# Kernel tuning notes

Measured on AMD Instinct MI355X. Metric: run time of the kernel, lower is better.

The kernel has to match this reference:

```python
import jax, jax.numpy as jnp
import numpy as np

N_NODES = 50000
N_EDGES = 800000
N_GRAPHS = 512
VOCAB = 100000
EMB = 64
HID = 128
CLASSES = 2


def setup_inputs() -> dict:
    key = jax.random.key(0)
    ks = jax.random.split(key, 12)
    x = jax.random.randint(ks[0], (N_NODES,), 0, VOCAB)
    edge_index = jax.random.randint(ks[1], (2, N_EDGES), 0, N_NODES)
    batch = jnp.sort(jax.random.randint(ks[2], (N_NODES,), 0, N_GRAPHS))
    s = lambda fan_in: 1.0 / np.sqrt(fan_in)
    emb_table = jax.random.normal(ks[3], (VOCAB, EMB), jnp.float32)
    w1_l = jax.random.uniform(ks[4], (EMB, HID), jnp.float32, -s(EMB), s(EMB))
    b1 = jnp.zeros((HID,), jnp.float32)
    w1_r = jax.random.uniform(ks[5], (EMB, HID), jnp.float32, -s(EMB), s(EMB))
    w2_l = jax.random.uniform(ks[6], (HID, HID), jnp.float32, -s(HID), s(HID))
    b2 = jnp.zeros((HID,), jnp.float32)
    w2_r = jax.random.uniform(ks[7], (HID, HID), jnp.float32, -s(HID), s(HID))
    w_out = jax.random.uniform(ks[8], (HID, CLASSES), jnp.float32, -s(HID), s(HID))
    b_out = jnp.zeros((CLASSES,), jnp.float32)
    return {"x": x, "edge_index": edge_index, "batch": batch,
            "emb_table": emb_table, "w1_l": w1_l, "b1": b1, "w1_r": w1_r,
            "w2_l": w2_l, "b2": b2, "w2_r": w2_r, "w_out": w_out, "b_out": b_out}


def _sage_conv(h, src, dst, w_l, b_l, w_r):
    # PyG SAGEConv (mean aggr): out = lin_l(mean_{j in N(i)} x_j) + lin_r(x_i)
    msg = h[src]                                              # [E, F] gather
    agg = jax.ops.segment_sum(msg, dst, num_segments=N_NODES)  # [N, F]
    deg = jax.ops.segment_sum(jnp.ones((src.shape[0],), h.dtype), dst,
                              num_segments=N_NODES)
    mean = agg / jnp.maximum(deg, 1.0)[:, None]
    return mean @ w_l + b_l + h @ w_r


def reference(x, edge_index, batch, emb_table, w1_l, b1, w1_r,
              w2_l, b2, w2_r, w_out, b_out):
    src, dst = edge_index[0], edge_index[1]
    h = emb_table[x]                                          # [N, EMB]
    h = jax.nn.relu(_sage_conv(h, src, dst, w1_l, b1, w1_r))
    # dropout is identity in eval mode
    h = jax.nn.relu(_sage_conv(h, src, dst, w2_l, b2, w2_r))
    # global mean pool over graphs
    pooled = jax.ops.segment_sum(h, batch, num_segments=N_GRAPHS)
    cnt = jax.ops.segment_sum(jnp.ones((N_NODES,), h.dtype), batch,
                              num_segments=N_GRAPHS)
    pooled = pooled / jnp.maximum(cnt, 1.0)[:, None]
    return pooled @ w_out + b_out                              # [G, CLASSES]
```

## Files before the change

kernel.cpp:

```cpp
#include <hip/hip_runtime.h>
#include <hip/hip_bf16.h>

#define N_NODES 50000
#define N_EDGES 800000
#define N_GRAPHS 512
#define EMB 64
#define HID 128

__device__ __forceinline__ unsigned f2bf(float f) {
    unsigned x = __float_as_uint(f);
    return (x + 0x7fffu + ((x >> 16) & 1u)) >> 16;
}
__device__ __forceinline__ unsigned packbf(float lo, float hi) {
    return f2bf(lo) | (f2bf(hi) << 16);
}
__device__ __forceinline__ float bf_lo(unsigned u) { return __uint_as_float(u << 16); }
__device__ __forceinline__ float bf_hi(unsigned u) { return __uint_as_float(u & 0xffff0000u); }

__global__ void k_embed_hist(const int* __restrict__ x, const float* __restrict__ emb,
                             const int* __restrict__ ei, float* __restrict__ h0,
                             uint2* __restrict__ h0b, int* __restrict__ deg) {
    int t = blockIdx.x * 256 + threadIdx.x;
    if (t >= N_EDGES) return;
    int n = t >> 4, c4 = t & 15;
    const float4* e4 = (const float4*)emb;
    float4 v = e4[(size_t)x[n] * 16 + c4];
    ((float4*)h0)[(size_t)n * 16 + c4] = v;
    uint2 b; b.x = packbf(v.x, v.y); b.y = packbf(v.z, v.w);
    h0b[(size_t)n * 16 + c4] = b;
    atomicAdd(&deg[ei[N_EDGES + t]], 1);
}

__global__ void k_scanA(const int* __restrict__ deg, int* __restrict__ rowptr,
                        int* __restrict__ bsums) {
    __shared__ int s[256];
    int t = threadIdx.x, i = blockIdx.x * 256 + t;
    int v = (i < N_NODES) ? deg[i] : 0;
    s[t] = v; __syncthreads();
    int xv = v;
    for (int off = 1; off < 256; off <<= 1) {
        int y = (t >= off) ? s[t - off] : 0;
        __syncthreads();
        xv += y; s[t] = xv;
        __syncthreads();
    }
    if (i < N_NODES) rowptr[i] = xv - v;
    if (t == 255) bsums[blockIdx.x] = xv;
}

__global__ void k_scanB(int* __restrict__ bsums, int nb) {
    __shared__ int s[256];
    int t = threadIdx.x;
    int v = (t < nb) ? bsums[t] : 0;
    s[t] = v; __syncthreads();
    int xv = v;
    for (int off = 1; off < 256; off <<= 1) {
        int y = (t >= off) ? s[t - off] : 0;
        __syncthreads();
        xv += y; s[t] = xv;
        __syncthreads();
    }
    if (t < nb) bsums[t] = xv - v;
}

__global__ void k_scanC(int* __restrict__ rowptr, int* __restrict__ wp,
                        const int* __restrict__ bsums) {
    int i = blockIdx.x * 256 + threadIdx.x;
    if (i < N_NODES) {
        int v = rowptr[i] + bsums[blockIdx.x];
        rowptr[i] = v;
        wp[i] = v;
    }
    if (i == 0) rowptr[N_NODES] = N_EDGES;
}

__global__ void k_scatter(const int* __restrict__ ei, int* __restrict__ wp,
                          int* __restrict__ nbr) {
    int e = blockIdx.x * 256 + threadIdx.x;
    if (e >= N_EDGES) return;
    int s = ei[e], d = ei[N_EDGES + e];
    int pos = atomicAdd(&wp[d], 1);
    nbr[pos] = s;
}

template <int F>
__device__ __forceinline__ void agg_tile_bf(const uint2* __restrict__ hb,
                                            const int* __restrict__ rowptr,
                                            const int* __restrict__ nbr,
                                            float* __restrict__ mean,
                                            int aggIdx, int t) {
    int wl = t >> 6;
    int l = t & 63;
    float4* m4 = (float4*)mean;

    int n, c;
    if constexpr (F == 128) { n = aggIdx * 16 + wl * 2 + (l >> 5); c = l & 31; }
    else                    { n = aggIdx * 32 + wl * 4 + (l >> 4); c = l & 15; }
    if (n >= N_NODES) return;
    constexpr int CU2 = F / 4;

    int r0 = rowptr[n], r1 = rowptr[n + 1];
    float inv = 1.0f / (float)max(r1 - r0, 1);

    float4 a[8];
    #pragma unroll
    for (int u = 0; u < 8; ++u) a[u] = make_float4(0.f, 0.f, 0.f, 0.f);

    int i = r0;
    for (; i + 7 < r1; i += 8) {
        int s0 = nbr[i + 0], s1 = nbr[i + 1], s2 = nbr[i + 2], s3 = nbr[i + 3];
        int s4 = nbr[i + 4], s5 = nbr[i + 5], s6 = nbr[i + 6], s7 = nbr[i + 7];
        uint2 v0 = hb[(size_t)s0 * CU2 + c];
        uint2 v1 = hb[(size_t)s1 * CU2 + c];
        uint2 v2 = hb[(size_t)s2 * CU2 + c];
        uint2 v3 = hb[(size_t)s3 * CU2 + c];
        uint2 v4 = hb[(size_t)s4 * CU2 + c];
        uint2 v5 = hb[(size_t)s5 * CU2 + c];
        uint2 v6 = hb[(size_t)s6 * CU2 + c];
        uint2 v7 = hb[(size_t)s7 * CU2 + c];
        a[0].x += bf_lo(v0.x); a[0].y += bf_hi(v0.x); a[0].z += bf_lo(v0.y); a[0].w += bf_hi(v0.y);
        a[1].x += bf_lo(v1.x); a[1].y += bf_hi(v1.x); a[1].z += bf_lo(v1.y); a[1].w += bf_hi(v1.y);
        a[2].x += bf_lo(v2.x); a[2].y += bf_hi(v2.x); a[2].z += bf_lo(v2.y); a[2].w += bf_hi(v2.y);
        a[3].x += bf_lo(v3.x); a[3].y += bf_hi(v3.x); a[3].z += bf_lo(v3.y); a[3].w += bf_hi(v3.y);
        a[4].x += bf_lo(v4.x); a[4].y += bf_hi(v4.x); a[4].z += bf_lo(v4.y); a[4].w += bf_hi(v4.y);
        a[5].x += bf_lo(v5.x); a[5].y += bf_hi(v5.x); a[5].z += bf_lo(v5.y); a[5].w += bf_hi(v5.y);
        a[6].x += bf_lo(v6.x); a[6].y += bf_hi(v6.x); a[6].z += bf_lo(v6.y); a[6].w += bf_hi(v6.y);
        a[7].x += bf_lo(v7.x); a[7].y += bf_hi(v7.x); a[7].z += bf_lo(v7.y); a[7].w += bf_hi(v7.y);
    }
    for (; i + 3 < r1; i += 4) {
        int s0 = nbr[i + 0], s1 = nbr[i + 1], s2 = nbr[i + 2], s3 = nbr[i + 3];
        uint2 v0 = hb[(size_t)s0 * CU2 + c];
        uint2 v1 = hb[(size_t)s1 * CU2 + c];
        uint2 v2 = hb[(size_t)s2 * CU2 + c];
        uint2 v3 = hb[(size_t)s3 * CU2 + c];
        a[0].x += bf_lo(v0.x); a[0].y += bf_hi(v0.x); a[0].z += bf_lo(v0.y); a[0].w += bf_hi(v0.y);
        a[1].x += bf_lo(v1.x); a[1].y += bf_hi(v1.x); a[1].z += bf_lo(v1.y); a[1].w += bf_hi(v1.y);
        a[2].x += bf_lo(v2.x); a[2].y += bf_hi(v2.x); a[2].z += bf_lo(v2.y); a[2].w += bf_hi(v2.y);
        a[3].x += bf_lo(v3.x); a[3].y += bf_hi(v3.x); a[3].z += bf_lo(v3.y); a[3].w += bf_hi(v3.y);
    }
    for (; i < r1; ++i) {
        uint2 v = hb[(size_t)nbr[i] * CU2 + c];
        a[0].x += bf_lo(v.x); a[0].y += bf_hi(v.x); a[0].z += bf_lo(v.y); a[0].w += bf_hi(v.y);
    }
    #pragma unroll
    for (int u = 1; u < 8; ++u) {
        a[0].x += a[u].x; a[0].y += a[u].y; a[0].z += a[u].z; a[0].w += a[u].w;
    }
    m4[(size_t)n * CU2 + c] = make_float4(a[0].x * inv, a[0].y * inv,
                                          a[0].z * inv, a[0].w * inv);
}

template <int K, bool MEAN, bool WB>
__device__ __forceinline__ void gemm_tile(const float* __restrict__ hin,
                                          const float* __restrict__ w,
                                          const float* __restrict__ bias,
                                          float* __restrict__ out,
                                          uint2* __restrict__ outb,
                                          int blk, int t, float* ls) {
    constexpr int LS = K + 2;
    constexpr int C4 = K / 4;
    int base = blk * 64;
    int lane = t & 63;
    int wid = __builtin_amdgcn_readfirstlane(t >> 6);
    int j0 = wid * 16;
    int node = base + lane;
    bool valid = node < N_NODES;

    const float4* h4 = (const float4*)hin;
    for (int idx = t; idx < 64 * C4; idx += 512) {
        int r = idx / C4, c4 = idx % C4;
        float4 v = (base + r < N_NODES) ? h4[(size_t)(base + r) * C4 + c4]
                                        : make_float4(0.f, 0.f, 0.f, 0.f);
        float* dp = &ls[r * LS + c4 * 4];
        dp[0] = v.x; dp[1] = v.y; dp[2] = v.z; dp[3] = v.w;
    }
    __syncthreads();

    float acc[16];
    if constexpr (MEAN) {
        const float4* o4 = (const float4*)out;
        #pragma unroll
        for (int jj = 0; jj < 4; ++jj) {
            float4 v = valid ? o4[(size_t)node * 32 + wid * 4 + jj]
                             : make_float4(0.f, 0.f, 0.f, 0.f);
            acc[jj * 4 + 0] = v.x; acc[jj * 4 + 1] = v.y;
            acc[jj * 4 + 2] = v.z; acc[jj * 4 + 3] = v.w;
        }
    } else {
        #pragma unroll
        for (int j = 0; j < 16; ++j) acc[j] = bias[j0 + j];
    }

    const float* lrow = &ls[lane * LS];
    #pragma unroll 4
    for (int k = 0; k < K; ++k) {
        float hv = lrow[k];
        const float* wk = &w[(size_t)k * 128 + j0];
        #pragma unroll
        for (int j = 0; j < 16; ++j) acc[j] = fmaf(hv, wk[j], acc[j]);
    }

    if (!valid) return;
    float4* o4 = (float4*)out;
    #pragma unroll
    for (int jj = 0; jj < 4; ++jj) {
        float4 v;
        if constexpr (MEAN) {
            v.x = fmaxf(acc[jj * 4 + 0], 0.f);
            v.y = fmaxf(acc[jj * 4 + 1], 0.f);
            v.z = fmaxf(acc[jj * 4 + 2], 0.f);
            v.w = fmaxf(acc[jj * 4 + 3], 0.f);
        } else {
            v.x = acc[jj * 4 + 0]; v.y = acc[jj * 4 + 1];
            v.z = acc[jj * 4 + 2]; v.w = acc[jj * 4 + 3];
        }
        o4[(size_t)node * 32 + wid * 4 + jj] = v;
        if constexpr (WB) {
            uint2 u; u.x = packbf(v.x, v.y); u.y = packbf(v.z, v.w);
            outb[(size_t)node * 32 + wid * 4 + jj] = u;
        }
    }
}

__global__ __launch_bounds__(512) void k_fuse1(
    const float* __restrict__ h0, const uint2* __restrict__ h0b,
    const int* __restrict__ rowptr, const int* __restrict__ nbr,
    float* __restrict__ mean1, const float* __restrict__ w1r,
    const float* __restrict__ b1, float* __restrict__ h1) {
    __shared__ float ls[64 * (64 + 2)];
    int b = blockIdx.x;
    if (b % 3 == 2)
        gemm_tile<64, false, false>(h0, w1r, b1, h1, nullptr, b / 3, threadIdx.x, ls);
    else
        agg_tile_bf<64>(h0b, rowptr, nbr, mean1, (b / 3) * 2 + b % 3, threadIdx.x);
}

__global__ __launch_bounds__(512) void k_fuse2(
    const float* __restrict__ h1, const uint2* __restrict__ h1b,
    const int* __restrict__ rowptr, const int* __restrict__ nbr,
    float* __restrict__ mean2, const float* __restrict__ w2r,
    const float* __restrict__ b2, float* __restrict__ h2) {
    __shared__ float ls[64 * (128 + 2)];
    int b = blockIdx.x;
    if (b % 5 == 4)
        gemm_tile<128, false, false>(h1, w2r, b2, h2, nullptr, b / 5, threadIdx.x, ls);
    else
        agg_tile_bf<128>(h1b, rowptr, nbr, mean2, (b / 5) * 4 + b % 5, threadIdx.x);
}

__global__ __launch_bounds__(512) void k_gemm_mean64(
    const float* __restrict__ mean1, const float* __restrict__ w1l,
    float* __restrict__ h1, uint2* __restrict__ h1b) {
    __shared__ float ls[64 * (64 + 2)];
    gemm_tile<64, true, true>(mean1, w1l, nullptr, h1, h1b, blockIdx.x, threadIdx.x, ls);
}

__global__ __launch_bounds__(512) void k_gemm_mean128(
    const float* __restrict__ mean2, const float* __restrict__ w2l,
    float* __restrict__ h2) {
    __shared__ float ls[64 * (128 + 2)];
    gemm_tile<128, true, false>(mean2, w2l, nullptr, h2, nullptr, blockIdx.x, threadIdx.x, ls);
}

__global__ void k_pool_head(const float* __restrict__ h2, const int* __restrict__ batch,
                            const float* __restrict__ w_out, const float* __restrict__ b_out,
                            float* __restrict__ out) {
    int g = blockIdx.x;
    int lo = 0, hi = N_NODES;
    while (lo < hi) { int mid = (lo + hi) >> 1; if (batch[mid] < g) lo = mid + 1; else hi = mid; }
    int s = lo;
    lo = s; hi = N_NODES;
    while (lo < hi) { int mid = (lo + hi) >> 1; if (batch[mid] < g + 1) lo = mid + 1; else hi = mid; }
    int e = lo;

    int f = threadIdx.x & 127, half = threadIdx.x >> 7;
    float acc = 0.0f;
    for (int r = s + half; r < e; r += 2) acc += h2[(size_t)r * 128 + f];
    __shared__ float tmp[256];
    tmp[threadIdx.x] = acc;
    __syncthreads();
    if (half == 0) {
        float p = (tmp[f] + tmp[f + 128]) / (float)max(e - s, 1);
        tmp[f]       = p * w_out[f * 2 + 0];
        tmp[f + 128] = p * w_out[f * 2 + 1];
    }
    __syncthreads();
    for (int str = 64; str > 0; str >>= 1) {
        if (threadIdx.x < str) {
            tmp[threadIdx.x] += tmp[threadIdx.x + str];
            tmp[threadIdx.x + 128] += tmp[threadIdx.x + 128 + str];
        }
        __syncthreads();
    }
    if (threadIdx.x == 0) {
        out[(size_t)g * 2 + 0] = tmp[0] + b_out[0];
        out[(size_t)g * 2 + 1] = tmp[128] + b_out[1];
    }
}

extern "C" void kernel_launch(void* const* d_in, const int* in_sizes, int n_in,
                              void* d_out, int out_size, void* d_ws, size_t ws_size,
                              hipStream_t stream) {
    const int*   x      = (const int*)d_in[0];
    const int*   ei     = (const int*)d_in[1];
    const int*   batch  = (const int*)d_in[2];
    const float* emb    = (const float*)d_in[3];
    const float* w1_l   = (const float*)d_in[4];
    const float* b1     = (const float*)d_in[5];
    const float* w1_r   = (const float*)d_in[6];
    const float* w2_l   = (const float*)d_in[7];
    const float* b2     = (const float*)d_in[8];
    const float* w2_r   = (const float*)d_in[9];
    const float* w_out  = (const float*)d_in[10];
    const float* b_out  = (const float*)d_in[11];
    float* out = (float*)d_out;

    float* F = (float*)d_ws;
    float* A = F;
    float* B = A + (size_t)N_NODES * 64;
    float* C = B + (size_t)N_NODES * 64;
    float* D = C + (size_t)N_NODES * 128;
    float* h0    = A;
    uint2* h1b   = (uint2*)A;
    float* mean1 = B;
    float* h1    = C;
    float* h2    = C;
    float* mean2 = D;
    uint2* h0b   = (uint2*)D;
    int*   deg   = (int*)(D + (size_t)N_NODES * 128);
    int*   rowptr= deg + N_NODES;
    int*   wp    = rowptr + N_NODES + 1;
    int*   nbr   = wp + N_NODES;
    int*   bsums = nbr + N_EDGES;

    const int NB = (N_NODES + 255) / 256;
    const int GB = (N_NODES + 63) / 64;

    hipMemsetAsync(deg, 0, (size_t)N_NODES * sizeof(int), stream);

    k_embed_hist<<<(N_EDGES + 255) / 256, 256, 0, stream>>>(x, emb, ei, h0, h0b, deg);
    k_scanA<<<NB, 256, 0, stream>>>(deg, rowptr, bsums);
    k_scanB<<<1, 256, 0, stream>>>(bsums, NB);
    k_scanC<<<NB, 256, 0, stream>>>(rowptr, wp, bsums);
    k_scatter<<<(N_EDGES + 255) / 256, 256, 0, stream>>>(ei, wp, nbr);

    k_fuse1<<<3 * GB, 512, 0, stream>>>(h0, h0b, rowptr, nbr, mean1, w1_r, b1, h1);
    k_gemm_mean64<<<GB, 512, 0, stream>>>(mean1, w1_l, h1, h1b);

    k_fuse2<<<5 * GB, 512, 0, stream>>>(h1, h1b, rowptr, nbr, mean2, w2_r, b2, h2);
    k_gemm_mean128<<<GB, 512, 0, stream>>>(mean2, w2_l, h2);

    k_pool_head<<<N_GRAPHS, 256, 0, stream>>>(h2, batch, w_out, b_out, out);

    (void)in_sizes; (void)n_in; (void)out_size; (void)ws_size;
}
```

Measured before the change: 370.2 us.

## Fuse mean-pool into final GEMM and drop fp32 activation copies

Removes the fp32 h0/h1 copies; self-term GEMMs now stage bf16 activations from shared memory. The layer-2 mean GEMM performs ReLU and a per-block segmented column sum into a pooled buffer with atomics, so h2 is never written or reread. The head kernel only normalizes and applies the output linear. This trades slightly lower precision on the root-term input and atomic contention for less global memory traffic.

```diff
diff --git a/kernel.cpp b/kernel.cpp
--- a/kernel.cpp
+++ b/kernel.cpp
@@ -18,14 +18,13 @@
 __device__ __forceinline__ float bf_hi(unsigned u) { return __uint_as_float(u & 0xffff0000u); }
 
 __global__ void k_embed_hist(const int* __restrict__ x, const float* __restrict__ emb,
-                             const int* __restrict__ ei, float* __restrict__ h0,
-                             uint2* __restrict__ h0b, int* __restrict__ deg) {
+                             const int* __restrict__ ei, uint2* __restrict__ h0b,
+                             int* __restrict__ deg) {
     int t = blockIdx.x * 256 + threadIdx.x;
     if (t >= N_EDGES) return;
     int n = t >> 4, c4 = t & 15;
     const float4* e4 = (const float4*)emb;
     float4 v = e4[(size_t)x[n] * 16 + c4];
-    ((float4*)h0)[(size_t)n * 16 + c4] = v;
     uint2 b; b.x = packbf(v.x, v.y); b.y = packbf(v.z, v.w);
     h0b[(size_t)n * 16 + c4] = b;
     atomicAdd(&deg[ei[N_EDGES + t]], 1);
@@ -150,48 +149,38 @@
                                           a[0].z * inv, a[0].w * inv);
 }
 
-template <int K, bool MEAN, bool WB>
-__device__ __forceinline__ void gemm_tile(const float* __restrict__ hin,
-                                          const float* __restrict__ w,
-                                          const float* __restrict__ bias,
-                                          float* __restrict__ out,
-                                          uint2* __restrict__ outb,
-                                          int blk, int t, float* ls) {
-    constexpr int LS = K + 2;
-    constexpr int C4 = K / 4;
-    int base = blk * 64;
-    int lane = t & 63;
-    int wid = __builtin_amdgcn_readfirstlane(t >> 6);
-    int j0 = wid * 16;
-    int node = base + lane;
-    bool valid = node < N_NODES;
-
+template <int K>
+__device__ __forceinline__ void stage_f32(const float* __restrict__ hin, int base,
+                                          int t, float* ls) {
+    constexpr int LS = K + 2, C4 = K / 4;
     const float4* h4 = (const float4*)hin;
     for (int idx = t; idx < 64 * C4; idx += 512) {
-        int r = idx / C4, c4 = idx % C4;
-        float4 v = (base + r < N_NODES) ? h4[(size_t)(base + r) * C4 + c4]
+        int r = idx / C4, c = idx % C4;
+        float4 v = (base + r < N_NODES) ? h4[(size_t)(base + r) * C4 + c]
                                         : make_float4(0.f, 0.f, 0.f, 0.f);
-        float* dp = &ls[r * LS + c4 * 4];
+        float* dp = &ls[r * LS + c * 4];
         dp[0] = v.x; dp[1] = v.y; dp[2] = v.z; dp[3] = v.w;
     }
-    __syncthreads();
-
-    float acc[16];
-    if constexpr (MEAN) {
-        const float4* o4 = (const float4*)out;
-        #pragma unroll
-        for (int jj = 0; jj < 4; ++jj) {
-            float4 v = valid ? o4[(size_t)node * 32 + wid * 4 + jj]
-                             : make_float4(0.f, 0.f, 0.f, 0.f);
-            acc[jj * 4 + 0] = v.x; acc[jj * 4 + 1] = v.y;
-            acc[jj * 4 + 2] = v.z; acc[jj * 4 + 3] = v.w;
-        }
-    } else {
-        #pragma unroll
-        for (int j = 0; j < 16; ++j) acc[j] = bias[j0 + j];
-    }
-
-    const float* lrow = &ls[lane * LS];
+}
+
+template <int K>
+__device__ __forceinline__ void stage_bf(const uint2* __restrict__ hb, int base,
+                                         int t, float* ls) {
+    constexpr int LS = K + 2, C2 = K / 4;
+    for (int idx = t; idx < 64 * C2; idx += 512) {
+        int r = idx / C2, c = idx % C2;
+        uint2 v = (base + r < N_NODES) ? hb[(size_t)(base + r) * C2 + c]
+                                       : make_uint2(0u, 0u);
+        float* dp = &ls[r * LS + c * 4];
+        dp[0] = bf_lo(v.x); dp[1] = bf_hi(v.x);
+        dp[2] = bf_lo(v.y); dp[3] = bf_hi(v.y);
+    }
+}
+
+template <int K>
+__device__ __forceinline__ void gemm_core(const float* __restrict__ lrow,
+                                          const float* __restrict__ w,
+                                          int j0, float (&acc)[16]) {
     #pragma unroll 4
     for (int k = 0; k < K; ++k) {
         float hv = lrow[k];
@@ -199,102 +188,160 @@
         #pragma unroll
         for (int j = 0; j < 16; ++j) acc[j] = fmaf(hv, wk[j], acc[j]);
     }
-
-    if (!valid) return;
-    float4* o4 = (float4*)out;
-    #pragma unroll
-    for (int jj = 0; jj < 4; ++jj) {
-        float4 v;
-        if constexpr (MEAN) {
-            v.x = fmaxf(acc[jj * 4 + 0], 0.f);
-            v.y = fmaxf(acc[jj * 4 + 1], 0.f);
-            v.z = fmaxf(acc[jj * 4 + 2], 0.f);
-            v.w = fmaxf(acc[jj * 4 + 3], 0.f);
-        } else {
-            v.x = acc[jj * 4 + 0]; v.y = acc[jj * 4 + 1];
-            v.z = acc[jj * 4 + 2]; v.w = acc[jj * 4 + 3];
+}
+
+__global__ __launch_bounds__(512) void k_fuse1(
+    const uint2* __restrict__ h0b, const int* __restrict__ rowptr,
+    const int* __restrict__ nbr, float* __restrict__ mean1,
+    const float* __restrict__ w1r, const float* __restrict__ b1,
+    float* __restrict__ pre1) {
+    __shared__ float ls[64 * 66];
+    int b = blockIdx.x, t = threadIdx.x;
+    if (b % 3 == 2) {
+        int base = (b / 3) * 64;
+        stage_bf<64>(h0b, base, t, ls);
+        __syncthreads();
+        int lane = t & 63, wid = __builtin_amdgcn_readfirstlane(t >> 6), j0 = wid * 16;
+        int node = base + lane;
+        float acc[16];
+        #pragma unroll
+        for (int j = 0; j < 16; ++j) acc[j] = b1[j0 + j];
+        gemm_core<64>(&ls[lane * 66], w1r, j0, acc);
+        if (node < N_NODES) {
+            float4* o4 = (float4*)pre1;
+            #pragma unroll
+            for (int jj = 0; jj < 4; ++jj)
+                o4[(size_t)node * 32 + wid * 4 + jj] =
+                    make_float4(acc[jj*4], acc[jj*4+1], acc[jj*4+2], acc[jj*4+3]);
         }
-        o4[(size_t)node * 32 + wid * 4 + jj] = v;
-        if constexpr (WB) {
-            uint2 u; u.x = packbf(v.x, v.y); u.y = packbf(v.z, v.w);
-            outb[(size_t)node * 32 + wid * 4 + jj] = u;
+    } else {
+        agg_tile_bf<64>(h0b, rowptr, nbr, mean1, (b / 3) * 2 + (b % 3), t);
+    }
+}
+
+__global__ __launch_bounds__(512) void k_fuse2(
+    const uint2* __restrict__ h1b, const int* __restrict__ rowptr,
+    const int* __restrict__ nbr, float* __restrict__ mean2,
+    const float* __restrict__ w2r, const float* __restrict__ b2,
+    float* __restrict__ pre2) {
+    __shared__ float ls[64 * 130];
+    int b = blockIdx.x, t = threadIdx.x;
+    if (b % 5 == 4) {
+        int base = (b / 5) * 64;
+        stage_bf<128>(h1b, base, t, ls);
+        __syncthreads();
+        int lane = t & 63, wid = __builtin_amdgcn_readfirstlane(t >> 6), j0 = wid * 16;
+        int node = base + lane;
+        float acc[16];
+        #pragma unroll
+        for (int j = 0; j < 16; ++j) acc[j] = b2[j0 + j];
+        gemm_core<128>(&ls[lane * 130], w2r, j0, acc);
+        if (node < N_NODES) {
+            float4* o4 = (float4*)pre2;
+            #pragma unroll
+            for (int jj = 0; jj < 4; ++jj)
+                o4[(size_t)node * 32 + wid * 4 + jj] =
+                    make_float4(acc[jj*4], acc[jj*4+1], acc[jj*4+2], acc[jj*4+3]);
         }
-    }
-}
-
-__global__ __launch_bounds__(512) void k_fuse1(
-    const float* __restrict__ h0, const uint2* __restrict__ h0b,
-    const int* __restrict__ rowptr, const int* __restrict__ nbr,
-    float* __restrict__ mean1, const float* __restrict__ w1r,
-    const float* __restrict__ b1, float* __restrict__ h1) {
-    __shared__ float ls[64 * (64 + 2)];
-    int b = blockIdx.x;
-    if (b % 3 == 2)
-        gemm_tile<64, false, false>(h0, w1r, b1, h1, nullptr, b / 3, threadIdx.x, ls);
-    else
-        agg_tile_bf<64>(h0b, rowptr, nbr, mean1, (b / 3) * 2 + b % 3, threadIdx.x);
-}
-
-__global__ __launch_bounds__(512) void k_fuse2(
-    const float* __restrict__ h1, const uint2* __restrict__ h1b,
-    const int* __restrict__ rowptr, const int* __restrict__ nbr,
-    float* __restrict__ mean2, const float* __restrict__ w2r,
-    const float* __restrict__ b2, float* __restrict__ h2) {
-    __shared__ float ls[64 * (128 + 2)];
-    int b = blockIdx.x;
-    if (b % 5 == 4)
-        gemm_tile<128, false, false>(h1, w2r, b2, h2, nullptr, b / 5, threadIdx.x, ls);
-    else
-        agg_tile_bf<128>(h1b, rowptr, nbr, mean2, (b / 5) * 4 + b % 5, threadIdx.x);
+    } else {
+        agg_tile_bf<128>(h1b, rowptr, nbr, mean2, (b / 5) * 4 + (b % 5), t);
+    }
 }
 
 __global__ __launch_bounds__(512) void k_gemm_mean64(
     const float* __restrict__ mean1, const float* __restrict__ w1l,
-    float* __restrict__ h1, uint2* __restrict__ h1b) {
-    __shared__ float ls[64 * (64 + 2)];
-    gemm_tile<64, true, true>(mean1, w1l, nullptr, h1, h1b, blockIdx.x, threadIdx.x, ls);
-}
-
-__global__ __launch_bounds__(512) void k_gemm_mean128(
+    const float* __restrict__ pre1, uint2* __restrict__ h1b) {
+    __shared__ float ls[64 * 66];
+    int t = threadIdx.x, base = blockIdx.x * 64;
+    stage_f32<64>(mean1, base, t, ls);
+    __syncthreads();
+    int lane = t & 63, wid = __builtin_amdgcn_readfirstlane(t >> 6), j0 = wid * 16;
+    int node = base + lane;
+    bool valid = node < N_NODES;
+    float acc[16];
+    const float4* p4 = (const float4*)pre1;
+    #pragma unroll
+    for (int jj = 0; jj < 4; ++jj) {
+        float4 v = valid ? p4[(size_t)node * 32 + wid * 4 + jj]
+                         : make_float4(0.f, 0.f, 0.f, 0.f);
+        acc[jj*4] = v.x; acc[jj*4+1] = v.y; acc[jj*4+2] = v.z; acc[jj*4+3] = v.w;
+    }
+    gemm_core<64>(&ls[lane * 66], w1l, j0, acc);
+    if (!valid) return;
+    #pragma unroll
+    for (int jj = 0; jj < 4; ++jj) {
+        float a0 = fmaxf(acc[jj*4+0], 0.f), a1 = fmaxf(acc[jj*4+1], 0.f);
+        float a2 = fmaxf(acc[jj*4+2], 0.f), a3 = fmaxf(acc[jj*4+3], 0.f);
+        uint2 u; u.x = packbf(a0, a1); u.y = packbf(a2, a3);
+        h1b[(size_t)node * 32 + wid * 4 + jj] = u;
+    }
+}
+
+__global__ __launch_bounds__(512) void k_mean128_pool(
     const float* __restrict__ mean2, const float* __restrict__ w2l,
-    float* __restrict__ h2) {
-    __shared__ float ls[64 * (128 + 2)];
-    gemm_tile<128, true, false>(mean2, w2l, nullptr, h2, nullptr, blockIdx.x, threadIdx.x, ls);
-}
-
-__global__ void k_pool_head(const float* __restrict__ h2, const int* __restrict__ batch,
-                            const float* __restrict__ w_out, const float* __restrict__ b_out,
-                            float* __restrict__ out) {
-    int g = blockIdx.x;
+    const float* __restrict__ pre2, const int* __restrict__ batch,
+    float* __restrict__ pooled) {
+    __shared__ float ls[64 * 130];
+    __shared__ int bb[64];
+    int t = threadIdx.x, base = blockIdx.x * 64;
+    stage_f32<128>(mean2, base, t, ls);
+    if (t < 64) bb[t] = (base + t < N_NODES) ? batch[base + t] : -1;
+    __syncthreads();
+    int lane = t & 63, wid = __builtin_amdgcn_readfirstlane(t >> 6), j0 = wid * 16;
+    int node = base + lane;
+    bool valid = node < N_NODES;
+    float acc[16];
+    const float4* p4 = (const float4*)pre2;
+    #pragma unroll
+    for (int jj = 0; jj < 4; ++jj) {
+        float4 v = valid ? p4[(size_t)node * 32 + wid * 4 + jj]
+                         : make_float4(0.f, 0.f, 0.f, 0.f);
+        acc[jj*4] = v.x; acc[jj*4+1] = v.y; acc[jj*4+2] = v.z; acc[jj*4+3] = v.w;
+    }
+    gemm_core<128>(&ls[lane * 130], w2l, j0, acc);
+    __syncthreads();
+    #pragma unroll
+    for (int j = 0; j < 16; ++j)
+        ls[lane * 129 + j0 + j] = valid ? fmaxf(acc[j], 0.f) : 0.f;
+    __syncthreads();
+    if (t < 128) {
+        int col = t;
+        float run = 0.f;
+        int gcur = bb[0];
+        for (int r = 0; r < 64; ++r) {
+            int g = bb[r];
+            if (g != gcur) {
+                if (gcur >= 0) atomicAdd(&pooled[gcur * 128 + col], run);
+                run = 0.f; gcur = g;
+            }
+            run += ls[r * 129 + col];
+        }
+        if (gcur >= 0) atomicAdd(&pooled[gcur * 128 + col], run);
+    }
+}
+
+__global__ void k_head(const float* __restrict__ pooled, const int* __restrict__ batch,
+                       const float* __restrict__ w_out, const float* __restrict__ b_out,
+                       float* __restrict__ out) {
+    int g = blockIdx.x, f = threadIdx.x;
     int lo = 0, hi = N_NODES;
-    while (lo < hi) { int mid = (lo + hi) >> 1; if (batch[mid] < g) lo = mid + 1; else hi = mid; }
+    while (lo < hi) { int m = (lo + hi) >> 1; if (batch[m] < g) lo = m + 1; else hi = m; }
     int s = lo;
     lo = s; hi = N_NODES;
-    while (lo < hi) { int mid = (lo + hi) >> 1; if (batch[mid] < g + 1) lo = mid + 1; else hi = mid; }
-    int e = lo;
-
-    int f = threadIdx.x & 127, half = threadIdx.x >> 7;
-    float acc = 0.0f;
-    for (int r = s + half; r < e; r += 2) acc += h2[(size_t)r * 128 + f];
-    __shared__ float tmp[256];
-    tmp[threadIdx.x] = acc;
+    while (lo < hi) { int m = (lo + hi) >> 1; if (batch[m] < g + 1) lo = m + 1; else hi = m; }
+    int cnt = lo - s;
+    float p = pooled[(size_t)g * 128 + f] / (float)max(cnt, 1);
+    __shared__ float red[256];
+    red[f] = p * w_out[f * 2 + 0];
+    red[128 + f] = p * w_out[f * 2 + 1];
     __syncthreads();
-    if (half == 0) {
-        float p = (tmp[f] + tmp[f + 128]) / (float)max(e - s, 1);
-        tmp[f]       = p * w_out[f * 2 + 0];
-        tmp[f + 128] = p * w_out[f * 2 + 1];
-    }
-    __syncthreads();
-    for (int str = 64; str > 0; str >>= 1) {
-        if (threadIdx.x < str) {
-            tmp[threadIdx.x] += tmp[threadIdx.x + str];
-            tmp[threadIdx.x + 128] += tmp[threadIdx.x + 128 + str];
-        }
-        __syncthreads();
-    }
-    if (threadIdx.x == 0) {
-        out[(size_t)g * 2 + 0] = tmp[0] + b_out[0];
-        out[(size_t)g * 2 + 1] = tmp[128] + b_out[1];
+    for (int st = 64; st > 0; st >>= 1) {
+        if (f < st) { red[f] += red[f + st]; red[128 + f] += red[128 + f + st]; }
+        __syncthreads();
+    }
+    if (f == 0) {
+        out[(size_t)g * 2 + 0] = red[0] + b_out[0];
+        out[(size_t)g * 2 + 1] = red[128] + b_out[1];
     }
 }
 
@@ -316,19 +363,15 @@
     float* out = (float*)d_out;
 
     float* F = (float*)d_ws;
-    float* A = F;
-    float* B = A + (size_t)N_NODES * 64;
-    float* C = B + (size_t)N_NODES * 64;
-    float* D = C + (size_t)N_NODES * 128;
-    float* h0    = A;
-    uint2* h1b   = (uint2*)A;
-    float* mean1 = B;
-    float* h1    = C;
-    float* h2    = C;
-    float* mean2 = D;
-    uint2* h0b   = (uint2*)D;
-    int*   deg   = (int*)(D + (size_t)N_NODES * 128);
-    int*   rowptr= deg + N_NODES;
+    float* mean1 = F;
+    uint2* h1b   = (uint2*)F;
+    float* pre1  = F + (size_t)N_NODES * 64;
+    float* pre2  = pre1;
+    float* mean2 = pre1 + (size_t)N_NODES * 128;
+    uint2* h0b   = (uint2*)(mean2 + (size_t)N_NODES * 128);
+    int*   deg   = (int*)((float*)h0b + (size_t)N_NODES * 32);
+    float* pooled= (float*)(deg + N_NODES);
+    int*   rowptr= (int*)(pooled + (size_t)N_GRAPHS * 128);
     int*   wp    = rowptr + N_NODES + 1;
     int*   nbr   = wp + N_NODES;
     int*   bsums = nbr + N_EDGES;
@@ -336,21 +379,22 @@
     const int NB = (N_NODES + 255) / 256;
     const int GB = (N_NODES + 63) / 64;
 
-    hipMemsetAsync(deg, 0, (size_t)N_NODES * sizeof(int), stream);
-
-    k_embed_hist<<<(N_EDGES + 255) / 256, 256, 0, stream>>>(x, emb, ei, h0, h0b, deg);
+    hipMemsetAsync(deg, 0, (size_t)N_NODES * sizeof(int)
+                          + (size_t)N_GRAPHS * 128 * sizeof(float), stream);
+
+    k_embed_hist<<<(N_EDGES + 255) / 256, 256, 0, stream>>>(x, emb, ei, h0b, deg);
     k_scanA<<<NB, 256, 0, stream>>>(deg, rowptr, bsums);
     k_scanB<<<1, 256, 0, stream>>>(bsums, NB);
     k_scanC<<<NB, 256, 0, stream>>>(rowptr, wp, bsums);
     k_scatter<<<(N_EDGES + 255) / 256, 256, 0, stream>>>(ei, wp, nbr);
 
-    k_fuse1<<<3 * GB, 512, 0, stream>>>(h0, h0b, rowptr, nbr, mean1, w1_r, b1, h1);
-    k_gemm_mean64<<<GB, 512, 0, stream>>>(mean1, w1_l, h1, h1b);
-
-    k_fuse2<<<5 * GB, 512, 0, stream>>>(h1, h1b, rowptr, nbr, mean2, w2_r, b2, h2);
-    k_gemm_mean128<<<GB, 512, 0, stream>>>(mean2, w2_l, h2);
-
-    k_pool_head<<<N_GRAPHS, 256, 0, stream>>>(h2, batch, w_out, b_out, out);
+    k_fuse1<<<3 * GB, 512, 0, stream>>>(h0b, rowptr, nbr, mean1, w1_r, b1, pre1);
+    k_gemm_mean64<<<GB, 512, 0, stream>>>(mean1, w1_l, pre1, h1b);
+
+    k_fuse2<<<5 * GB, 512, 0, stream>>>(h1b, rowptr, nbr, mean2, w2_r, b2, pre2);
+    k_mean128_pool<<<GB, 512, 0, stream>>>(mean2, w2_l, pre2, batch, pooled);
+
+    k_head<<<N_GRAPHS, 128, 0, stream>>>(pooled, batch, w_out, b_out, out);
 
     (void)in_sizes; (void)n_in; (void)out_size; (void)ws_size;
 }
```

After: 332.8 us. 10.1% less time.
